# Kernel optimization log

Hardware: AMD Instinct MI355X
Metric: run time of the kernel (lower is better)

## Reference

```python
import jax, jax.numpy as jnp
import numpy as np
from jax import lax

SEQ, BATCH, FEAT = 64, 32768, 15
H1 = H2 = H3 = 4  # hidden sizes from the source module


def setup_inputs() -> dict:
    key = jax.random.key(0)
    ks = jax.random.split(key, 11)
    s = 0.1
    return {
        "x": jax.random.normal(ks[0], (SEQ, BATCH, FEAT), jnp.float32),
        "w1": jax.random.normal(ks[1], (H1, FEAT), jnp.float32) * s,
        "b1": jax.random.normal(ks[2], (H1,), jnp.float32) * s,
        "w2": jax.random.normal(ks[3], (H2, H1), jnp.float32) * s,
        "b2": jax.random.normal(ks[4], (H2,), jnp.float32) * s,
        "w_ih": jax.random.normal(ks[5], (4 * H3, H2), jnp.float32) * s,
        "w_hh": jax.random.normal(ks[6], (4 * H3, H3), jnp.float32) * s,
        "b_ih": jax.random.normal(ks[7], (4 * H3,), jnp.float32) * s,
        "b_hh": jax.random.normal(ks[8], (4 * H3,), jnp.float32) * s,
        "w3": jax.random.normal(ks[9], (1, H3), jnp.float32) * s,
        "b3": jax.random.normal(ks[10], (1,), jnp.float32) * s,
    }


def reference(x, w1, b1, w2, b2, w_ih, w_hh, b_ih, b_hh, w3, b3):
    seq, batch, _ = x.shape
    hidden = w_hh.shape[1]
    # front-end MLP: fc1 -> relu -> fc2 -> sigmoid   (applied per timestep)
    h1 = jax.nn.relu(jnp.einsum('sbf,hf->sbh', x, w1) + b1)          # [S,B,H1]
    h2 = jax.nn.sigmoid(jnp.einsum('sbh,gh->sbg', h1, w2) + b2)      # [S,B,H2]
    # precompute input-to-gate projections for all timesteps: [S,B,4H]
    gx = jnp.einsum('sbh,gh->sbg', h2, w_ih) + b_ih + b_hh

    def step(carry, gxt):
        h, c = carry
        gates = gxt + h @ w_hh.T                                      # [B,4H]
        i, f, g, o = jnp.split(gates, 4, axis=-1)                     # torch order i,f,g,o
        i = jax.nn.sigmoid(i)
        f = jax.nn.sigmoid(f)
        g = jnp.tanh(g)
        o = jax.nn.sigmoid(o)
        c = f * c + i * g
        h = o * jnp.tanh(c)
        return (h, c), None

    h0 = jnp.zeros((batch, hidden), x.dtype)
    c0 = jnp.zeros((batch, hidden), x.dtype)
    (h_last, _), _ = lax.scan(step, (h0, c0), gx)                     # last-step hidden [B,H3]
    out = jax.nn.sigmoid(h_last @ w3.T + b3)                          # [B,1]
    return out.reshape(batch)
```

## Files before the change

### kernel.cpp

```cpp
#include <hip/hip_runtime.h>

#define SEQ   64
#define BATCH 32768
#define FEAT  15
#define SLAB  (BATCH * FEAT)

#define LOG2E 1.4426950408889634f

__device__ __forceinline__ float fast_rcp(float x)  { return __builtin_amdgcn_rcpf(x); }
__device__ __forceinline__ float ex2(float x)       { return __builtin_amdgcn_exp2f(x); }

template <int CTRL>
__device__ __forceinline__ float qmov(float v) {
    return __int_as_float(
        __builtin_amdgcn_mov_dpp(__float_as_int(v), CTRL, 0xf, 0xf, false));
}

struct __attribute__((aligned(4))) F4 { float a, b, c, d; };
__device__ __forceinline__ F4 ldf4(const float* p) { return *(const F4*)p; }

__global__ __launch_bounds__(256, 2) void lstm_fused(
    const float* __restrict__ x,
    const float* __restrict__ w1,  const float* __restrict__ b1,
    const float* __restrict__ w2,  const float* __restrict__ b2,
    const float* __restrict__ wih, const float* __restrict__ whh,
    const float* __restrict__ bih, const float* __restrict__ bhh,
    const float* __restrict__ w3,  const float* __restrict__ b3,
    float* __restrict__ out)
{
    const int tid = threadIdx.x;
    const int w   = tid >> 6;
    const int l   = tid & 63;
    const int u   = l & 3;
    const int e   = l >> 2;
    const int elem = blockIdx.x * 64 + w * 16 + e;

    const int qoff = (u == 3) ? 11 : 4 * u;
    const float* xp = x + (size_t)elem * FEAT + qoff;

    float W1[FEAT], W2[4], WI[16], WH[16], BI[4];
#pragma unroll
    for (int f = 0; f < FEAT; ++f) W1[f] = w1[u * FEAT + f];
    const float B1v = b1[u];
#pragma unroll
    for (int j = 0; j < 4; ++j) W2[j] = -LOG2E * w2[u * 4 + j];
    const float B2v = -LOG2E * b2[u];
#pragma unroll
    for (int g = 0; g < 4; ++g) {
        const float sg = (g == 2) ? (2.0f * LOG2E) : -LOG2E;
#pragma unroll
        for (int j = 0; j < 4; ++j) {
            WI[g * 4 + j] = sg * wih[(g * 4 + u) * 4 + j];
            WH[g * 4 + j] = sg * whh[(g * 4 + u) * 4 + j];
        }
        BI[g] = sg * (bih[g * 4 + u] + bhh[g * 4 + u]);
    }
    const float W3v = -LOG2E * w3[u];
    const float B3v = -LOG2E * b3[0];

    float h = 0.0f, c = 0.0f;

    auto step = [&](F4 q) {
        float xv[FEAT];
        xv[0]  = qmov<0x00>(q.a); xv[1]  = qmov<0x00>(q.b);
        xv[2]  = qmov<0x00>(q.c); xv[3]  = qmov<0x00>(q.d);
        xv[4]  = qmov<0x55>(q.a); xv[5]  = qmov<0x55>(q.b);
        xv[6]  = qmov<0x55>(q.c); xv[7]  = qmov<0x55>(q.d);
        xv[8]  = qmov<0xAA>(q.a); xv[9]  = qmov<0xAA>(q.b);
        xv[10] = qmov<0xAA>(q.c); xv[11] = qmov<0xAA>(q.d);
        xv[12] = qmov<0xFF>(q.b); xv[13] = qmov<0xFF>(q.c);
        xv[14] = qmov<0xFF>(q.d);
        float a0 = B1v, a1 = 0.0f, a2 = 0.0f;
#pragma unroll
        for (int f = 0; f < 5; ++f) a0 = fmaf(W1[f],      xv[f],      a0);
#pragma unroll
        for (int f = 0; f < 5; ++f) a1 = fmaf(W1[5 + f],  xv[5 + f],  a1);
#pragma unroll
        for (int f = 0; f < 5; ++f) a2 = fmaf(W1[10 + f], xv[10 + f], a2);
        const float h1 = fmaxf(a0 + (a1 + a2), 0.0f);
        float q0 = qmov<0x00>(h1), q1 = qmov<0x55>(h1), q2 = qmov<0xAA>(h1), q3 = qmov<0xFF>(h1);
        const float a2n = fmaf(W2[0], q0, fmaf(W2[1], q1, fmaf(W2[2], q2, fmaf(W2[3], q3, B2v))));
        const float h2 = fast_rcp(1.0f + ex2(a2n));
        q0 = qmov<0x00>(h2); q1 = qmov<0x55>(h2); q2 = qmov<0xAA>(h2); q3 = qmov<0xFF>(h2);
        float gi = fmaf(WI[0],  q0, fmaf(WI[1],  q1, fmaf(WI[2],  q2, fmaf(WI[3],  q3, BI[0]))));
        float gf = fmaf(WI[4],  q0, fmaf(WI[5],  q1, fmaf(WI[6],  q2, fmaf(WI[7],  q3, BI[1]))));
        float gg = fmaf(WI[8],  q0, fmaf(WI[9],  q1, fmaf(WI[10], q2, fmaf(WI[11], q3, BI[2]))));
        float go = fmaf(WI[12], q0, fmaf(WI[13], q1, fmaf(WI[14], q2, fmaf(WI[15], q3, BI[3]))));
        q0 = qmov<0x00>(h); q1 = qmov<0x55>(h); q2 = qmov<0xAA>(h); q3 = qmov<0xFF>(h);
        gi = fmaf(WH[0],  q0, fmaf(WH[1],  q1, fmaf(WH[2],  q2, fmaf(WH[3],  q3, gi))));
        gf = fmaf(WH[4],  q0, fmaf(WH[5],  q1, fmaf(WH[6],  q2, fmaf(WH[7],  q3, gf))));
        gg = fmaf(WH[8],  q0, fmaf(WH[9],  q1, fmaf(WH[10], q2, fmaf(WH[11], q3, gg))));
        go = fmaf(WH[12], q0, fmaf(WH[13], q1, fmaf(WH[14], q2, fmaf(WH[15], q3, go))));
        const float ig = fast_rcp(1.0f + ex2(gi));
        const float fg = fast_rcp(1.0f + ex2(gf));
        const float og = fast_rcp(1.0f + ex2(go));
        const float gt = fmaf(-2.0f, fast_rcp(1.0f + ex2(gg)), 1.0f);
        c = fmaf(fg, c, ig * gt);
        const float tc = fmaf(-2.0f, fast_rcp(1.0f + ex2(c * (2.0f * LOG2E))), 1.0f);
        h = og * tc;
    };

    F4 Qa[8], Qb[8];
    auto prefetch8 = [&](F4* Q, const float* base) {
#pragma unroll
        for (int j = 0; j < 8; ++j) Q[j] = ldf4(base + (size_t)j * SLAB);
    };
    auto compute8 = [&](F4* Q) {
#pragma unroll
        for (int j = 0; j < 8; ++j) step(Q[j]);
    };

    prefetch8(Qa, xp);
#pragma unroll 1
    for (int i = 0; i < 3; ++i) {
        const float* bft = xp + (size_t)(16 * i + 8) * SLAB;
        prefetch8(Qb, bft);
        __builtin_amdgcn_sched_barrier(0);
        compute8(Qa);
        prefetch8(Qa, bft + (size_t)8 * SLAB);
        __builtin_amdgcn_sched_barrier(0);
        compute8(Qb);
    }
    prefetch8(Qb, xp + (size_t)56 * SLAB);
    __builtin_amdgcn_sched_barrier(0);
    compute8(Qa);
    compute8(Qb);

    float p = W3v * h;
    p += qmov<0xB1>(p);
    p += qmov<0x4E>(p);
    if (u == 0) out[elem] = fast_rcp(1.0f + ex2(p + B3v));
}

extern "C" void kernel_launch(void* const* d_in, const int* in_sizes, int n_in,
                              void* d_out, int out_size, void* d_ws, size_t ws_size,
                              hipStream_t stream) {
    (void)in_sizes; (void)n_in; (void)d_ws; (void)ws_size; (void)out_size;
    const float* x   = (const float*)d_in[0];
    const float* w1  = (const float*)d_in[1];
    const float* b1  = (const float*)d_in[2];
    const float* w2  = (const float*)d_in[3];
    const float* b2  = (const float*)d_in[4];
    const float* wih = (const float*)d_in[5];
    const float* whh = (const float*)d_in[6];
    const float* bih = (const float*)d_in[7];
    const float* bhh = (const float*)d_in[8];
    const float* w3  = (const float*)d_in[9];
    const float* b3  = (const float*)d_in[10];
    float* out = (float*)d_out;

    lstm_fused<<<dim3(512), dim3(256), 0, stream>>>(
        x, w1, b1, w2, b2, wih, whh, bih, bhh, w3, b3, out);
}
```

Baseline: 35.46 us.

## Use packed FMA and per-quad partial dot products for LSTM step math

Each of the four lanes in a quad now computes partial fc1 dot products over only its own four loaded features for all four hidden units, then reduces them across the quad with DPP adds. This replaces broadcasting all 15 features to every lane. The gate projections and the fc1 partials use two-wide float vectors so the compiler can emit packed FMA instructions, cutting the VALU instruction count per step. In exchange each step gains extra horizontal adds and DPP reductions. The load also changes from an aligned struct to four scalar loads, which may change how the loads vectorize.

```diff
diff --git a/kernel.cpp b/kernel.cpp
--- a/kernel.cpp
+++ b/kernel.cpp
@@ -7,8 +7,11 @@
 
 #define LOG2E 1.4426950408889634f
 
-__device__ __forceinline__ float fast_rcp(float x)  { return __builtin_amdgcn_rcpf(x); }
-__device__ __forceinline__ float ex2(float x)       { return __builtin_amdgcn_exp2f(x); }
+typedef float v2f __attribute__((ext_vector_type(2)));
+
+__device__ __forceinline__ float fast_rcp(float x) { return __builtin_amdgcn_rcpf(x); }
+__device__ __forceinline__ float ex2(float x)      { return __builtin_amdgcn_exp2f(x); }
+__device__ __forceinline__ float sig2(float t)     { return fast_rcp(1.0f + ex2(t)); }
 
 template <int CTRL>
 __device__ __forceinline__ float qmov(float v) {
@@ -16,8 +19,9 @@
         __builtin_amdgcn_mov_dpp(__float_as_int(v), CTRL, 0xf, 0xf, false));
 }
 
-struct __attribute__((aligned(4))) F4 { float a, b, c, d; };
-__device__ __forceinline__ F4 ldf4(const float* p) { return *(const F4*)p; }
+__device__ __forceinline__ v2f fma2(v2f a, v2f b, v2f c) { return a * b + c; }
+
+struct Fq { float a, b, c, d; };
 
 __global__ __launch_bounds__(256, 2) void lstm_fused(
     const float* __restrict__ x,
@@ -38,74 +42,80 @@
     const int qoff = (u == 3) ? 11 : 4 * u;
     const float* xp = x + (size_t)elem * FEAT + qoff;
 
-    float W1[FEAT], W2[4], WI[16], WH[16], BI[4];
+    v2f W1a[4], W1b[4], SE[4];
 #pragma unroll
-    for (int f = 0; f < FEAT; ++f) W1[f] = w1[u * FEAT + f];
-    const float B1v = b1[u];
+    for (int j = 0; j < 4; ++j) {
+        const float* r = w1 + j * FEAT + qoff;
+        W1a[j] = v2f{(u == 3) ? 0.0f : r[0], r[1]};
+        W1b[j] = v2f{r[2], r[3]};
+        SE[j]  = v2f{(u == 0) ? b1[j] : 0.0f, 0.0f};
+    }
+    float W2s[4];
 #pragma unroll
-    for (int j = 0; j < 4; ++j) W2[j] = -LOG2E * w2[u * 4 + j];
+    for (int j = 0; j < 4; ++j) W2s[j] = -LOG2E * w2[u * 4 + j];
     const float B2v = -LOG2E * b2[u];
+    v2f WIp[4][2], WHp[4][2], BIg[4];
 #pragma unroll
     for (int g = 0; g < 4; ++g) {
         const float sg = (g == 2) ? (2.0f * LOG2E) : -LOG2E;
-#pragma unroll
-        for (int j = 0; j < 4; ++j) {
-            WI[g * 4 + j] = sg * wih[(g * 4 + u) * 4 + j];
-            WH[g * 4 + j] = sg * whh[(g * 4 + u) * 4 + j];
-        }
-        BI[g] = sg * (bih[g * 4 + u] + bhh[g * 4 + u]);
+        const int row = (g * 4 + u) * 4;
+        WIp[g][0] = v2f{sg * wih[row + 0], sg * wih[row + 1]};
+        WIp[g][1] = v2f{sg * wih[row + 2], sg * wih[row + 3]};
+        WHp[g][0] = v2f{sg * whh[row + 0], sg * whh[row + 1]};
+        WHp[g][1] = v2f{sg * whh[row + 2], sg * whh[row + 3]};
+        BIg[g]    = v2f{sg * (bih[g * 4 + u] + bhh[g * 4 + u]), 0.0f};
     }
     const float W3v = -LOG2E * w3[u];
     const float B3v = -LOG2E * b3[0];
 
     float h = 0.0f, c = 0.0f;
 
-    auto step = [&](F4 q) {
-        float xv[FEAT];
-        xv[0]  = qmov<0x00>(q.a); xv[1]  = qmov<0x00>(q.b);
-        xv[2]  = qmov<0x00>(q.c); xv[3]  = qmov<0x00>(q.d);
-        xv[4]  = qmov<0x55>(q.a); xv[5]  = qmov<0x55>(q.b);
-        xv[6]  = qmov<0x55>(q.c); xv[7]  = qmov<0x55>(q.d);
-        xv[8]  = qmov<0xAA>(q.a); xv[9]  = qmov<0xAA>(q.b);
-        xv[10] = qmov<0xAA>(q.c); xv[11] = qmov<0xAA>(q.d);
-        xv[12] = qmov<0xFF>(q.b); xv[13] = qmov<0xFF>(q.c);
-        xv[14] = qmov<0xFF>(q.d);
-        float a0 = B1v, a1 = 0.0f, a2 = 0.0f;
+    auto step = [&](Fq q) {
+        const v2f f01 = v2f{q.a, q.b}, f23 = v2f{q.c, q.d};
+        float P[4];
 #pragma unroll
-        for (int f = 0; f < 5; ++f) a0 = fmaf(W1[f],      xv[f],      a0);
+        for (int j = 0; j < 4; ++j) {
+            const v2f p2 = fma2(W1a[j], f01, fma2(W1b[j], f23, SE[j]));
+            P[j] = p2.x + p2.y;
+        }
 #pragma unroll
-        for (int f = 0; f < 5; ++f) a1 = fmaf(W1[5 + f],  xv[5 + f],  a1);
+        for (int j = 0; j < 4; ++j) {
+            P[j] += qmov<0xB1>(P[j]);
+            P[j] += qmov<0x4E>(P[j]);
+            P[j] = fmaxf(P[j], 0.0f);
+        }
+        const float a2n = fmaf(W2s[0], P[0], fmaf(W2s[1], P[1],
+                          fmaf(W2s[2], P[2], fmaf(W2s[3], P[3], B2v))));
+        const float h2 = sig2(a2n);
+        const v2f q01 = v2f{qmov<0x00>(h2), qmov<0x55>(h2)};
+        const v2f q23 = v2f{qmov<0xAA>(h2), qmov<0xFF>(h2)};
+        v2f A[4];
 #pragma unroll
-        for (int f = 0; f < 5; ++f) a2 = fmaf(W1[10 + f], xv[10 + f], a2);
-        const float h1 = fmaxf(a0 + (a1 + a2), 0.0f);
-        float q0 = qmov<0x00>(h1), q1 = qmov<0x55>(h1), q2 = qmov<0xAA>(h1), q3 = qmov<0xFF>(h1);
-        const float a2n = fmaf(W2[0], q0, fmaf(W2[1], q1, fmaf(W2[2], q2, fmaf(W2[3], q3, B2v))));
-        const float h2 = fast_rcp(1.0f + ex2(a2n));
-        q0 = qmov<0x00>(h2); q1 = qmov<0x55>(h2); q2 = qmov<0xAA>(h2); q3 = qmov<0xFF>(h2);
-        float gi = fmaf(WI[0],  q0, fmaf(WI[1],  q1, fmaf(WI[2],  q2, fmaf(WI[3],  q3, BI[0]))));
-        float gf = fmaf(WI[4],  q0, fmaf(WI[5],  q1, fmaf(WI[6],  q2, fmaf(WI[7],  q3, BI[1]))));
-        float gg = fmaf(WI[8],  q0, fmaf(WI[9],  q1, fmaf(WI[10], q2, fmaf(WI[11], q3, BI[2]))));
-        float go = fmaf(WI[12], q0, fmaf(WI[13], q1, fmaf(WI[14], q2, fmaf(WI[15], q3, BI[3]))));
-        q0 = qmov<0x00>(h); q1 = qmov<0x55>(h); q2 = qmov<0xAA>(h); q3 = qmov<0xFF>(h);
-        gi = fmaf(WH[0],  q0, fmaf(WH[1],  q1, fmaf(WH[2],  q2, fmaf(WH[3],  q3, gi))));
-        gf = fmaf(WH[4],  q0, fmaf(WH[5],  q1, fmaf(WH[6],  q2, fmaf(WH[7],  q3, gf))));
-        gg = fmaf(WH[8],  q0, fmaf(WH[9],  q1, fmaf(WH[10], q2, fmaf(WH[11], q3, gg))));
-        go = fmaf(WH[12], q0, fmaf(WH[13], q1, fmaf(WH[14], q2, fmaf(WH[15], q3, go))));
-        const float ig = fast_rcp(1.0f + ex2(gi));
-        const float fg = fast_rcp(1.0f + ex2(gf));
-        const float og = fast_rcp(1.0f + ex2(go));
-        const float gt = fmaf(-2.0f, fast_rcp(1.0f + ex2(gg)), 1.0f);
+        for (int g = 0; g < 4; ++g)
+            A[g] = fma2(WIp[g][0], q01, fma2(WIp[g][1], q23, BIg[g]));
+        const v2f h01 = v2f{qmov<0x00>(h), qmov<0x55>(h)};
+        const v2f h23 = v2f{qmov<0xAA>(h), qmov<0xFF>(h)};
+#pragma unroll
+        for (int g = 0; g < 4; ++g)
+            A[g] = fma2(WHp[g][0], h01, fma2(WHp[g][1], h23, A[g]));
+        const float ig = sig2(A[0].x + A[0].y);
+        const float fg = sig2(A[1].x + A[1].y);
+        const float gt = fmaf(-2.0f, sig2(A[2].x + A[2].y), 1.0f);
+        const float og = sig2(A[3].x + A[3].y);
         c = fmaf(fg, c, ig * gt);
-        const float tc = fmaf(-2.0f, fast_rcp(1.0f + ex2(c * (2.0f * LOG2E))), 1.0f);
+        const float tc = fmaf(-2.0f, sig2(c * (2.0f * LOG2E)), 1.0f);
         h = og * tc;
     };
 
-    F4 Qa[8], Qb[8];
-    auto prefetch8 = [&](F4* Q, const float* base) {
+    Fq Qa[8], Qb[8];
+    auto ld4 = [](const float* p) {
+        Fq r; r.a = p[0]; r.b = p[1]; r.c = p[2]; r.d = p[3]; return r;
+    };
+    auto prefetch8 = [&](Fq* Q, const float* base) {
 #pragma unroll
-        for (int j = 0; j < 8; ++j) Q[j] = ldf4(base + (size_t)j * SLAB);
+        for (int j = 0; j < 8; ++j) Q[j] = ld4(base + (size_t)j * SLAB);
     };
-    auto compute8 = [&](F4* Q) {
+    auto compute8 = [&](Fq* Q) {
 #pragma unroll
         for (int j = 0; j < 8; ++j) step(Q[j]);
     };
@@ -129,7 +139,7 @@
     float p = W3v * h;
     p += qmov<0xB1>(p);
     p += qmov<0x4E>(p);
-    if (u == 0) out[elem] = fast_rcp(1.0f + ex2(p + B3v));
+    if (u == 0) out[elem] = sig2(p + B3v);
 }
 
 extern "C" void kernel_launch(void* const* d_in, const int* in_sizes, int n_in,
```

Measured after the change: 33.50 us. -5.5%, faster.
